# Kernel optimization log

Hardware: AMD Instinct MI355X
Metric: run time of the kernel (lower is better)

## Reference

```python
import jax, jax.numpy as jnp
import numpy as np
from jax import lax

B, F, T, H = 32, 1024, 512, 64
ENC_SIZES = [2*F+1, 1387, 726, H]      # linear interp 2049 -> 64, depth 3
DEC_SIZES = [F+H+1, 1067, 1046, F]     # linear interp 1089 -> 1024, depth 3


def _mlp(ws, bs, x):
    # fully connected stack, ReLU between layers, no final activation
    n = len(ws)
    for i in range(n):
        x = x @ ws[i] + bs[i]
        if i < n - 1:
            x = jax.nn.relu(x)
    return x


def setup_inputs() -> dict:
    key = jax.random.key(0)
    ks = jax.random.split(key, 8)
    d = {"x": jax.random.normal(ks[0], (B, F, T), dtype=jnp.float32)}
    for i, (fin, fout) in enumerate(zip(ENC_SIZES[:-1], ENC_SIZES[1:])):
        d[f"ew{i}"] = jax.random.normal(ks[1+i], (fin, fout), jnp.float32) / np.sqrt(fin)
        d[f"eb{i}"] = jnp.zeros((fout,), jnp.float32)
    for i, (fin, fout) in enumerate(zip(DEC_SIZES[:-1], DEC_SIZES[1:])):
        d[f"dw{i}"] = jax.random.normal(ks[4+i], (fin, fout), jnp.float32) / np.sqrt(fin)
        d[f"db{i}"] = jnp.zeros((fout,), jnp.float32)
    return d


def reference(x, ew0, eb0, ew1, eb1, ew2, eb2, dw0, db0, dw1, db1, dw2, db2):
    enc_w, enc_b = (ew0, ew1, ew2), (eb0, eb1, eb2)
    dec_w, dec_b = (dw0, dw1, dw2), (db0, db1, db2)
    b = x.shape[0]
    xs = jnp.moveaxis(x, 2, 0)                       # [T, B, F]
    ts = (jnp.arange(T, dtype=x.dtype) / T)          # [T]

    # ---- encode: prev_stft feedback recurrence ----
    def enc_step(prev_stft, inp):
        curr, tval = inp
        tcol = jnp.full((b, 1), tval, dtype=x.dtype)
        comb = jnp.concatenate([prev_stft, curr, tcol], axis=1)  # [B, 2F+1]
        h = _mlp(enc_w, enc_b, comb)                             # [B, H]
        return curr, h

    _, hs = lax.scan(enc_step, jnp.zeros((b, F), x.dtype), (xs, ts))
    # flatten(-2) then view(B,H,T) round-trips, so keep [T,B,H]; tanh applied after flatten
    hiddens = jnp.tanh(hs)                           # [T, B, H]

    # ---- decode: prev_stft = decoder output recurrence ----
    def dec_step(prev_stft, inp):
        h_t, tval = inp
        tcol = jnp.full((b, 1), tval, dtype=x.dtype)
        comb = jnp.concatenate([h_t, prev_stft, tcol], axis=1)   # [B, H+F+1]
        out = _mlp(dec_w, dec_b, comb)                           # [B, F]
        return out, out

    _, ys = lax.scan(dec_step, jnp.zeros((b, F), x.dtype), (hiddens, ts))
    return jnp.transpose(ys, (1, 2, 0))              # [B, F, T]
```

## Files before the change

### kernel.cpp

```cpp
#include <hip/hip_runtime.h>
#include <hip/hip_bf16.h>
#include <hip/hip_fp16.h>


typedef _Float16 f16x8 __attribute__((ext_vector_type(8)));
typedef float f32x4 __attribute__((ext_vector_type(4)));
typedef unsigned short u16;
typedef unsigned int u32;
typedef unsigned long long u64;

#define MFMA(a, b, c) __builtin_amdgcn_mfma_f32_16x16x32_f16((a), (b), (c), 0, 0, 0)

__device__ __forceinline__ float h2f(u16 u) { __half h; __builtin_memcpy(&h, &u, 2); return __half2float(h); }
__device__ __forceinline__ u16 f2h(float f) { __half h = __float2half(f); u16 u; __builtin_memcpy(&u, &h, 2); return u; }

__device__ __forceinline__ void st_act4(u32* p, u32 v) {
  __hip_atomic_store(p, v, __ATOMIC_RELAXED, __HIP_MEMORY_SCOPE_AGENT);
}
__device__ __forceinline__ f16x8 ld_act16(const u16* p) {
  u64 lo = __hip_atomic_load((const u64*)p, __ATOMIC_RELAXED, __HIP_MEMORY_SCOPE_AGENT);
  u64 hi = __hip_atomic_load((const u64*)(p + 4), __ATOMIC_RELAXED, __HIP_MEMORY_SCOPE_AGENT);
  union { u64 q[2]; f16x8 v; } u;
  u.q[0] = lo; u.q[1] = hi;
  return u.v;
}

__global__ __launch_bounds__(256) void zero_u16_kernel(u16* p, int n) {
  int i = blockIdx.x * 256 + threadIdx.x;
  if (i < n) p[i] = 0;
}
__global__ __launch_bounds__(256) void zero_u32_kernel(int* p, int n) {
  int i = blockIdx.x * 256 + threadIdx.x;
  if (i < n) p[i] = 0;
}
__global__ __launch_bounds__(256) void zpad_kernel(u16* p) {
  int id = blockIdx.x * 256 + threadIdx.x;
  int row = id >> 4, col = 1072 + (id & 15);
  p[(size_t)row * 1088 + col] = 0;
}

__global__ __launch_bounds__(256) void transpose_kernel(const float* __restrict__ x, u16* __restrict__ xT) {
  __shared__ float tile[64][65];
  int b = blockIdx.z, f0 = blockIdx.x * 64, t0 = blockIdx.y * 64;
  const float* xp = x + (size_t)b * (1024 * 512);
  for (int rep = 0; rep < 16; ++rep) {
    int e = rep * 256 + threadIdx.x;
    int fi = e >> 6, tj = e & 63;
    tile[fi][tj] = xp[(size_t)(f0 + fi) * 512 + t0 + tj];
  }
  __syncthreads();
  for (int rep = 0; rep < 16; ++rep) {
    int e = rep * 256 + threadIdx.x;
    int tj = e >> 6, fi = e & 63;
    xT[(size_t)((t0 + tj + 1) * 32 + b) * 1024 + f0 + fi] = f2h(tile[fi][tj]);
  }
}

__global__ __launch_bounds__(256) void pack_w_kernel(const float* __restrict__ W, int ldw, int row0,
                                                     int Kr, int Nr, u16* __restrict__ out, int Np, int total) {
  int id = blockIdx.x * 256 + threadIdx.x;
  if (id >= total) return;
  int kq = id / Np, n = id % Np;
  union { u16 v[8]; uint4 q; } un;
#pragma unroll
  for (int j = 0; j < 8; ++j) {
    int k = kq * 8 + j;
    float f = (k < Kr && n < Nr) ? W[(size_t)(row0 + k) * ldw + n] : 0.f;
    un.v[j] = f2h(f);
  }
  *(uint4*)(out + (size_t)id * 8) = un.q;
}

__global__ __launch_bounds__(256) void c2x_kernel(const float* __restrict__ dw0, const float* __restrict__ db2,
                                                  float* __restrict__ c2x) {
  int n = blockIdx.x * 256 + threadIdx.x;
  if (n >= 1152) return;
  float s = 0.f;
  if (n < 1067) {
    for (int k = 0; k < 1024; ++k) s += db2[k] * dw0[(size_t)(64 + k) * 1067 + n];
  }
  c2x[n] = s;
}

__global__ __launch_bounds__(256) void cvt_a_kernel(const float* __restrict__ src, u16* __restrict__ dst) {
  int i = blockIdx.x * 256 + threadIdx.x;
  int r = i >> 10;
  dst[i] = f2h(r < 1046 ? src[i] : 0.f);
}

template <int TWOSRC, int ACT, int T1, int T2, int PACKO>
__global__ __launch_bounds__(256) void gemm_kernel(
    const u16* __restrict__ A, int lda,
    const u16* __restrict__ Wp, int Np,
    const float* __restrict__ bias, int nb,
    const float* __restrict__ wt1, int nw1,
    const float* __restrict__ wt2, int nw2,
    u16* __restrict__ out, int ldo, int Kp) {
  __shared__ u16 As[128][72];
  __shared__ u16 Bs[8 * 64 * 8];
  const int tid = threadIdx.x;
  const int bx = blockIdx.x, by = blockIdx.y;
  const int m0 = by * 128, n0 = bx * 64;
  const int l = tid & 63, wv = tid >> 6, lm = l & 15, lg = l >> 4;
  f32x4 acc[2][4] = {};
  for (int k0 = 0; k0 < Kp; k0 += 64) {
#pragma unroll
    for (int c = 0; c < 4; ++c) {
      int idx = c * 256 + tid;
      int row = idx >> 3, seg = idx & 7;
      int kk = k0 + seg * 8;
      const u16* ap;
      if (TWOSRC) {
        int half = (kk >= 1024) ? 1 : 0;
        ap = A + (size_t)(m0 + row + half * 32) * lda + (kk - half * 1024);
      } else {
        ap = A + (size_t)(m0 + row) * lda + kk;
      }
      *(uint4*)&As[row][seg * 8] = *(const uint4*)ap;
    }
#pragma unroll
    for (int c = 0; c < 2; ++c) {
      int idx = c * 256 + tid;
      int e0 = idx * 8;
      int kq = e0 >> 9, inner = e0 & 511;
      const u16* gp = Wp + (size_t)((k0 >> 3) + kq) * (Np * 8) + n0 * 8 + inner;
      *(uint4*)(Bs + e0) = *(const uint4*)gp;
    }
    __syncthreads();
#pragma unroll
    for (int ks = 0; ks < 2; ++ks) {
      f16x8 af0 = *(const f16x8*)&As[wv * 32 + lm][ks * 32 + lg * 8];
      f16x8 af1 = *(const f16x8*)&As[wv * 32 + 16 + lm][ks * 32 + lg * 8];
#pragma unroll
      for (int nf = 0; nf < 4; ++nf) {
        f16x8 bfr = *(const f16x8*)(Bs + ((ks * 4 + lg) * 64 + nf * 16 + lm) * 8);
        acc[0][nf] = MFMA(af0, bfr, acc[0][nf]);
        acc[1][nf] = MFMA(af1, bfr, acc[1][nf]);
      }
    }
    __syncthreads();
  }
#pragma unroll
  for (int mr = 0; mr < 2; ++mr) {
    int rb = m0 + wv * 32 + mr * 16;
    int tt = rb >> 5;
#pragma unroll
    for (int nf = 0; nf < 4; ++nf) {
      int col = n0 + nf * 16 + lm;
      float bv = (col < nb) ? bias[col] : 0.f;
      if (T1) bv += (float)tt * (1.f / 512.f) * ((col < nw1) ? wt1[col] : 0.f);
      if (T2) bv += ((tt > 0) ? 1.f : 0.f) * ((col < nw2) ? wt2[col] : 0.f);
#pragma unroll
      for (int v = 0; v < 4; ++v) {
        float xv = acc[mr][nf][v] + bv;
        if (ACT == 1) xv = fmaxf(xv, 0.f);
        if (ACT == 2) xv = tanhf(xv);
        if (PACKO) {
          int r = rb + lg * 4 + v;
          out[((size_t)(r >> 3) * Np + col) * 8 + (r & 7)] = f2h(xv);
        } else {
          out[(size_t)(rb + lg * 4 + v) * ldo + col] = f2h(xv);
        }
      }
    }
  }
}

#define NWG 67

__device__ __forceinline__ void gbar(int* flags, int bid, int tid, int gen) {
  asm volatile("s_waitcnt vmcnt(0)" ::: "memory");
  __syncthreads();
  if (tid == 0)
    __hip_atomic_store(flags + bid * 32, gen, __ATOMIC_RELAXED, __HIP_MEMORY_SCOPE_AGENT);
  if (tid < NWG) {
    while (__hip_atomic_load(flags + tid * 32, __ATOMIC_RELAXED, __HIP_MEMORY_SCOPE_AGENT) < gen)
      __builtin_amdgcn_s_sleep(1);
  }
  __syncthreads();
}

__device__ __forceinline__ void dec_mm(const u16* __restrict__ in, const u16* wl,
                                       float (*red)[512], int tid, int lm, int lg, int wv,
                                       int e0, float& s0, float& s1) {
  const int kq0 = wv * 36;
  f32x4 acc0 = {}, acc1 = {};
#pragma unroll
  for (int ks = 0; ks < 9; ++ks) {
    int kq = kq0 + ks * 4 + lg;
    const u16* pa = in + kq * 256 + lm * 8;
    f16x8 a0f = ld_act16(pa);
    f16x8 a1f = ld_act16(pa + 128);
    f16x8 bf = *(const f16x8*)(wl + ((size_t)kq * 16 + lm) * 8);
    acc0 = MFMA(a0f, bf, acc0);
    acc1 = MFMA(a1f, bf, acc1);
  }
  __syncthreads();
#pragma unroll
  for (int v = 0; v < 4; ++v) {
    red[wv][(lg * 4 + v) * 16 + lm] = acc0[v];
    red[wv][(16 + lg * 4 + v) * 16 + lm] = acc1[v];
  }
  __syncthreads();
  s0 = red[0][e0] + red[1][e0] + red[2][e0] + red[3][e0];
  s1 = red[0][e0 + 1] + red[1][e0 + 1] + red[2][e0 + 1] + red[3][e0 + 1];
}

__global__ __launch_bounds__(256, 1) void decoder_kernel(
    const u16* __restrict__ W1p, const u16* __restrict__ Mp,
    const u16* __restrict__ hpart, const float* __restrict__ db1,
    u16* a0, u16* a1, u16* __restrict__ a1buf, int* flags) {
  __shared__ __align__(16) u16 wlds[2 * 2304 * 8];
  __shared__ float red[4][512];
  const int tid = threadIdx.x, bid = blockIdx.x;
  const int l = tid & 63, wv = tid >> 6, lm = l & 15, lg = l >> 4;
  const int n0 = bid * 16;
  for (int i = tid; i < 2 * 2304; i += 256) {
    int layer = i / 2304, rem = i % 2304, kq = rem >> 4, c = rem & 15;
    const u16* base = (layer == 0) ? W1p : Mp;
    *(uint4*)(wlds + (size_t)i * 8) = *(const uint4*)(base + ((size_t)kq * 1152 + n0 + c) * 8);
  }
  const int e0 = tid * 2, row = e0 >> 4, c0 = e0 & 15, na = n0 + c0;
  u32* a0slot = (u32*)(a0 + (((size_t)(na >> 3) * 32 + row) * 8 + (na & 7)));
  u32* a1slot = (u32*)(a1 + (((size_t)(na >> 3) * 32 + row) * 8 + (na & 7)));
  int gen = 0;
  {
    u32 pk = *(const u32*)(hpart + row * 1152 + na);
    float s0 = fmaxf(h2f((u16)(pk & 0xffff)), 0.f);
    float s1 = fmaxf(h2f((u16)(pk >> 16)), 0.f);
    st_act4(a0slot, (u32)f2h(s0) | ((u32)f2h(s1) << 16));
  }
  gbar(flags, bid, tid, ++gen);
#pragma unroll 1
  for (int t = 0; t < 512; ++t) {
    float bv0 = (na < 1046) ? db1[na] : 0.f;
    float bv1 = (na + 1 < 1046) ? db1[na + 1] : 0.f;
    float s0, s1;
    dec_mm(a0, wlds, red, tid, lm, lg, wv, e0, s0, s1);
    s0 = fmaxf(s0 + bv0, 0.f);
    s1 = fmaxf(s1 + bv1, 0.f);
    u32 opk = (u32)f2h(s0) | ((u32)f2h(s1) << 16);
    st_act4(a1slot, opk);
    __builtin_nontemporal_store(opk, (u32*)(a1buf + ((size_t)(t * 32 + row) * 1088 + na)));
    gbar(flags, bid, tid, ++gen);
    if (t < 511) {
      u32 pk = *(const u32*)(hpart + (size_t)(t + 1) * 36864 + row * 1152 + na);
      dec_mm(a1, wlds + 2304 * 8, red, tid, lm, lg, wv, e0, s0, s1);
      s0 = fmaxf(s0 + h2f((u16)(pk & 0xffff)), 0.f);
      s1 = fmaxf(s1 + h2f((u16)(pk >> 16)), 0.f);
      st_act4(a0slot, (u32)f2h(s0) | ((u32)f2h(s1) << 16));
      gbar(flags, bid, tid, ++gen);
    }
  }
}

__global__ __launch_bounds__(256) void finalize_kernel(const u16* __restrict__ ytmp,
                                                       float* __restrict__ dout) {
  __shared__ float tile[64][65];
  int b = blockIdx.z, n0 = blockIdx.x * 64, t0 = blockIdx.y * 64;
  for (int rep = 0; rep < 16; ++rep) {
    int e = rep * 256 + threadIdx.x;
    int tt = e >> 6, nn = e & 63;
    tile[tt][nn] = h2f(ytmp[(size_t)((t0 + tt) * 32 + b) * 1024 + n0 + nn]);
  }
  __syncthreads();
  for (int rep = 0; rep < 16; ++rep) {
    int e = rep * 256 + threadIdx.x;
    int nn = e >> 6, tt = e & 63;
    dout[((size_t)b * 1024 + n0 + nn) * 512 + t0 + tt] = tile[tt][nn];
  }
}

extern "C" void kernel_launch(void* const* d_in, const int* in_sizes, int n_in,
                              void* d_out, int out_size, void* d_ws, size_t ws_size,
                              hipStream_t stream) {
  (void)in_sizes; (void)n_in; (void)out_size; (void)ws_size;
  const float* x   = (const float*)d_in[0];
  const float* ew0 = (const float*)d_in[1];
  const float* eb0 = (const float*)d_in[2];
  const float* ew1 = (const float*)d_in[3];
  const float* eb1 = (const float*)d_in[4];
  const float* ew2 = (const float*)d_in[5];
  const float* eb2 = (const float*)d_in[6];
  const float* dw0 = (const float*)d_in[7];
  const float* db0 = (const float*)d_in[8];
  const float* dw1 = (const float*)d_in[9];
  const float* db1 = (const float*)d_in[10];
  const float* dw2 = (const float*)d_in[11];
  const float* db2 = (const float*)d_in[12];

  char* ws = (char*)d_ws;
  u16* xT    = (u16*)(ws + 0);
  u16* ytmp  = (u16*)(ws + 0);
  u16* act2  = (u16*)(ws + 33619968ull);
  u16* A16   = (u16*)(ws + 33619968ull);
  u16* Mp    = (u16*)(ws + 33619968ull + 2359296ull);
  int* flags = (int*)(ws + 33619968ull + 8388608ull);
  u16* hid   = (u16*)(ws + 58785792ull);
  u16* hpart = (u16*)(ws + 60882944ull);
  u16* We0p  = (u16*)(ws + 98631680ull);
  u16* We1p  = (u16*)(ws + 104398848ull);
  u16* We2p  = (u16*)(ws + 106561536ull);
  u16* Wh0p  = (u16*)(ws + 106659840ull);
  u16* Wd0p  = (u16*)(ws + 106807296ull);
  u16* Wd1p  = (u16*)(ws + 109461504ull);
  u16* Wd2p  = (u16*)(ws + 112115712ull);
  float* c2x = (float*)(ws + 114769920ull);
  u16* a0    = (u16*)(ws + 114774528ull);
  u16* a1    = (u16*)(ws + 114848256ull);

  u16* act1  = (u16*)d_out;
  u16* a1buf = (u16*)d_out;
  float* dout = (float*)d_out;

  zero_u16_kernel<<<dim3(128), dim3(256), 0, stream>>>(xT, 32 * 1024);
  zero_u16_kernel<<<dim3(288), dim3(256), 0, stream>>>(a0, 2 * 36864);

  transpose_kernel<<<dim3(16, 8, 32), dim3(256), 0, stream>>>(x, xT);

  pack_w_kernel<<<dim3(1408), dim3(256), 0, stream>>>(ew0, 1387, 0, 2048, 1387, We0p, 1408, 256 * 1408);
  pack_w_kernel<<<dim3(528),  dim3(256), 0, stream>>>(ew1, 726, 0, 1387, 726, We1p, 768, 176 * 768);
  pack_w_kernel<<<dim3(24),   dim3(256), 0, stream>>>(ew2, 64, 0, 726, 64, We2p, 64, 96 * 64);
  pack_w_kernel<<<dim3(36),   dim3(256), 0, stream>>>(dw0, 1067, 0, 64, 1067, Wh0p, 1152, 8 * 1152);
  pack_w_kernel<<<dim3(648),  dim3(256), 0, stream>>>(dw0, 1067, 64, 1024, 1067, Wd0p, 1152, 144 * 1152);
  pack_w_kernel<<<dim3(648),  dim3(256), 0, stream>>>(dw1, 1046, 0, 1067, 1046, Wd1p, 1152, 144 * 1152);
  pack_w_kernel<<<dim3(648),  dim3(256), 0, stream>>>(dw2, 1024, 0, 1046, 1024, Wd2p, 1152, 144 * 1152);

  c2x_kernel<<<dim3(5), dim3(256), 0, stream>>>(dw0, db2, c2x);

  gemm_kernel<1, 1, 1, 0, 0><<<dim3(22, 128), dim3(256), 0, stream>>>(
      xT, 1024, We0p, 1408, eb0, 1387, ew0 + (size_t)2048 * 1387, 1387, nullptr, 0, act1, 1408, 2048);
  gemm_kernel<0, 1, 0, 0, 0><<<dim3(12, 128), dim3(256), 0, stream>>>(
      act1, 1408, We1p, 768, eb1, 726, nullptr, 0, nullptr, 0, act2, 768, 1408);
  gemm_kernel<0, 2, 0, 0, 0><<<dim3(1, 128), dim3(256), 0, stream>>>(
      act2, 768, We2p, 64, eb2, 64, nullptr, 0, nullptr, 0, hid, 64, 768);
  gemm_kernel<0, 0, 1, 1, 0><<<dim3(18, 128), dim3(256), 0, stream>>>(
      hid, 64, Wh0p, 1152, db0, 1067, dw0 + (size_t)1088 * 1067, 1067, c2x, 1152, hpart, 1152, 64);

  cvt_a_kernel<<<dim3(4608), dim3(256), 0, stream>>>(dw2, A16);
  gemm_kernel<0, 0, 0, 0, 1><<<dim3(18, 9), dim3(256), 0, stream>>>(
      A16, 1024, Wd0p, 1152, nullptr, 0, nullptr, 0, nullptr, 0, Mp, 0, 1024);

  zero_u32_kernel<<<dim3(9), dim3(256), 0, stream>>>(flags, NWG * 32);
  zpad_kernel<<<dim3(1024), dim3(256), 0, stream>>>(a1buf);

  decoder_kernel<<<dim3(NWG), dim3(256), 0, stream>>>(Wd1p, Mp, hpart, db1, a0, a1, a1buf, flags);

  gemm_kernel<0, 0, 0, 0, 0><<<dim3(16, 128), dim3(256), 0, stream>>>(
      a1buf, 1088, Wd2p, 1152, db2, 1024, nullptr, 0, nullptr, 0, ytmp, 1024, 1088);
  finalize_kernel<<<dim3(16, 8, 32), dim3(256), 0, stream>>>(ytmp, dout);
}
```

Baseline: 3.766 ms.

## Split decoder recurrence into two independent batch-half chains with smaller barriers

The persistent decoder kernel now runs two independent chains, one per half of the batch (16 rows each), on 68 workgroups. Each workgroup handles 32 output columns instead of 16, and each chain synchronises only its own 34 workgroups through a separate flag set. This is meant to cut grid-barrier latency on the serial 512-step recurrence by shrinking each barrier's participant count, at the cost of more weight data per workgroup in LDS. The a1buf store is no longer nontemporal, and the zero-padding and activation-zeroing launches are removed. Removing those launches may leave padding columns 1072-1087 of a1buf or the activation buffers uninitialised.

```diff
diff --git a/kernel.cpp b/kernel.cpp
--- a/kernel.cpp
+++ b/kernel.cpp
@@ -32,11 +32,6 @@
 __global__ __launch_bounds__(256) void zero_u32_kernel(int* p, int n) {
   int i = blockIdx.x * 256 + threadIdx.x;
   if (i < n) p[i] = 0;
-}
-__global__ __launch_bounds__(256) void zpad_kernel(u16* p) {
-  int id = blockIdx.x * 256 + threadIdx.x;
-  int row = id >> 4, col = 1072 + (id & 15);
-  p[(size_t)row * 1088 + col] = 0;
 }
 
 __global__ __launch_bounds__(256) void transpose_kernel(const float* __restrict__ x, u16* __restrict__ xT) {
@@ -166,91 +161,99 @@
   }
 }
 
-#define NWG 67
-
-__device__ __forceinline__ void gbar(int* flags, int bid, int tid, int gen) {
+#define NWGD 68
+#define NWGC 34
+
+__device__ __forceinline__ void gbar(int* cf, int wgc, int tid, int gen) {
   asm volatile("s_waitcnt vmcnt(0)" ::: "memory");
   __syncthreads();
   if (tid == 0)
-    __hip_atomic_store(flags + bid * 32, gen, __ATOMIC_RELAXED, __HIP_MEMORY_SCOPE_AGENT);
-  if (tid < NWG) {
-    while (__hip_atomic_load(flags + tid * 32, __ATOMIC_RELAXED, __HIP_MEMORY_SCOPE_AGENT) < gen)
+    __hip_atomic_store(cf + wgc * 4, gen, __ATOMIC_RELAXED, __HIP_MEMORY_SCOPE_AGENT);
+  if (tid < NWGC) {
+    while (__hip_atomic_load(cf + tid * 4, __ATOMIC_RELAXED, __HIP_MEMORY_SCOPE_AGENT) < gen)
       __builtin_amdgcn_s_sleep(1);
   }
   __syncthreads();
 }
 
-__device__ __forceinline__ void dec_mm(const u16* __restrict__ in, const u16* wl,
-                                       float (*red)[512], int tid, int lm, int lg, int wv,
-                                       int e0, float& s0, float& s1) {
+__device__ __forceinline__ void dec_mm32(const u16* __restrict__ in, const u16* wl,
+                                         float (*red)[512], int lm, int lg, int wv) {
   const int kq0 = wv * 36;
-  f32x4 acc0 = {}, acc1 = {};
+  f32x4 accA = {}, accB = {};
 #pragma unroll
   for (int ks = 0; ks < 9; ++ks) {
     int kq = kq0 + ks * 4 + lg;
-    const u16* pa = in + kq * 256 + lm * 8;
-    f16x8 a0f = ld_act16(pa);
-    f16x8 a1f = ld_act16(pa + 128);
-    f16x8 bf = *(const f16x8*)(wl + ((size_t)kq * 16 + lm) * 8);
-    acc0 = MFMA(a0f, bf, acc0);
-    acc1 = MFMA(a1f, bf, acc1);
+    f16x8 af = ld_act16(in + (size_t)kq * 128 + lm * 8);
+    f16x8 b0 = *(const f16x8*)(wl + ((size_t)kq * 32 + lm) * 8);
+    f16x8 b1 = *(const f16x8*)(wl + ((size_t)kq * 32 + 16 + lm) * 8);
+    accA = MFMA(af, b0, accA);
+    accB = MFMA(af, b1, accB);
   }
   __syncthreads();
 #pragma unroll
   for (int v = 0; v < 4; ++v) {
-    red[wv][(lg * 4 + v) * 16 + lm] = acc0[v];
-    red[wv][(16 + lg * 4 + v) * 16 + lm] = acc1[v];
-  }
-  __syncthreads();
-  s0 = red[0][e0] + red[1][e0] + red[2][e0] + red[3][e0];
-  s1 = red[0][e0 + 1] + red[1][e0 + 1] + red[2][e0 + 1] + red[3][e0 + 1];
+    red[wv][(lg * 4 + v) * 32 + lm] = accA[v];
+    red[wv][(lg * 4 + v) * 32 + 16 + lm] = accB[v];
+  }
+  __syncthreads();
 }
 
 __global__ __launch_bounds__(256, 1) void decoder_kernel(
     const u16* __restrict__ W1p, const u16* __restrict__ Mp,
     const u16* __restrict__ hpart, const float* __restrict__ db1,
-    u16* a0, u16* a1, u16* __restrict__ a1buf, int* flags) {
-  __shared__ __align__(16) u16 wlds[2 * 2304 * 8];
+    u16* actbase, u16* __restrict__ a1buf, int* flags) {
+  __shared__ __align__(16) u16 w1lds[144 * 32 * 8];
+  __shared__ __align__(16) u16 mlds[144 * 32 * 8];
   __shared__ float red[4][512];
   const int tid = threadIdx.x, bid = blockIdx.x;
+  const int chain = bid & 1, wgc = bid >> 1;
+  const int n0 = wgc * 32;
   const int l = tid & 63, wv = tid >> 6, lm = l & 15, lg = l >> 4;
-  const int n0 = bid * 16;
-  for (int i = tid; i < 2 * 2304; i += 256) {
-    int layer = i / 2304, rem = i % 2304, kq = rem >> 4, c = rem & 15;
-    const u16* base = (layer == 0) ? W1p : Mp;
-    *(uint4*)(wlds + (size_t)i * 8) = *(const uint4*)(base + ((size_t)kq * 1152 + n0 + c) * 8);
-  }
-  const int e0 = tid * 2, row = e0 >> 4, c0 = e0 & 15, na = n0 + c0;
-  u32* a0slot = (u32*)(a0 + (((size_t)(na >> 3) * 32 + row) * 8 + (na & 7)));
-  u32* a1slot = (u32*)(a1 + (((size_t)(na >> 3) * 32 + row) * 8 + (na & 7)));
+  for (int i = tid; i < 144 * 32; i += 256) {
+    int kq = i >> 5, c = i & 31;
+    *(uint4*)(w1lds + (size_t)i * 8) = *(const uint4*)(W1p + ((size_t)kq * 1152 + n0 + c) * 8);
+    *(uint4*)(mlds + (size_t)i * 8) = *(const uint4*)(Mp + ((size_t)kq * 1152 + n0 + c) * 8);
+  }
+  u16* a0 = actbase + (size_t)chain * 2 * 18432;
+  u16* a1 = a0 + 18432;
+  int* cf = flags + chain * 512;
+  const int e0 = tid * 2;
+  const int erow = e0 >> 5, ecol = e0 & 31;
+  const int na = n0 + ecol;
+  const int hrow = chain * 16 + erow;
+  u32* a0slot = (u32*)(a0 + ((size_t)(na >> 3) * 128 + (size_t)erow * 8 + (na & 7)));
+  u32* a1slot = (u32*)(a1 + ((size_t)(na >> 3) * 128 + (size_t)erow * 8 + (na & 7)));
+  const float bv0 = (na < 1046) ? db1[na] : 0.f;
+  const float bv1 = (na + 1 < 1046) ? db1[na + 1] : 0.f;
   int gen = 0;
+  __syncthreads();
   {
-    u32 pk = *(const u32*)(hpart + row * 1152 + na);
+    u32 pk = *(const u32*)(hpart + (size_t)hrow * 1152 + na);
     float s0 = fmaxf(h2f((u16)(pk & 0xffff)), 0.f);
     float s1 = fmaxf(h2f((u16)(pk >> 16)), 0.f);
     st_act4(a0slot, (u32)f2h(s0) | ((u32)f2h(s1) << 16));
   }
-  gbar(flags, bid, tid, ++gen);
+  gbar(cf, wgc, tid, ++gen);
 #pragma unroll 1
   for (int t = 0; t < 512; ++t) {
-    float bv0 = (na < 1046) ? db1[na] : 0.f;
-    float bv1 = (na + 1 < 1046) ? db1[na + 1] : 0.f;
-    float s0, s1;
-    dec_mm(a0, wlds, red, tid, lm, lg, wv, e0, s0, s1);
-    s0 = fmaxf(s0 + bv0, 0.f);
-    s1 = fmaxf(s1 + bv1, 0.f);
+    dec_mm32(a0, w1lds, red, lm, lg, wv);
+    float s0 = red[0][e0] + red[1][e0] + red[2][e0] + red[3][e0] + bv0;
+    float s1 = red[0][e0 + 1] + red[1][e0 + 1] + red[2][e0 + 1] + red[3][e0 + 1] + bv1;
+    s0 = fmaxf(s0, 0.f);
+    s1 = fmaxf(s1, 0.f);
     u32 opk = (u32)f2h(s0) | ((u32)f2h(s1) << 16);
     st_act4(a1slot, opk);
-    __builtin_nontemporal_store(opk, (u32*)(a1buf + ((size_t)(t * 32 + row) * 1088 + na)));
-    gbar(flags, bid, tid, ++gen);
-    if (t < 511) {
-      u32 pk = *(const u32*)(hpart + (size_t)(t + 1) * 36864 + row * 1152 + na);
-      dec_mm(a1, wlds + 2304 * 8, red, tid, lm, lg, wv, e0, s0, s1);
-      s0 = fmaxf(s0 + h2f((u16)(pk & 0xffff)), 0.f);
-      s1 = fmaxf(s1 + h2f((u16)(pk >> 16)), 0.f);
-      st_act4(a0slot, (u32)f2h(s0) | ((u32)f2h(s1) << 16));
-      gbar(flags, bid, tid, ++gen);
-    }
+    *(u32*)(a1buf + ((size_t)(t * 32 + hrow) * 1088 + na)) = opk;
+    u32 hpk = 0;
+    if (t < 511)
+      hpk = *(const u32*)(hpart + (size_t)(t + 1) * 36864 + (size_t)hrow * 1152 + na);
+    gbar(cf, wgc, tid, ++gen);
+    if (t == 511) break;
+    dec_mm32(a1, mlds, red, lm, lg, wv);
+    float r0 = red[0][e0] + red[1][e0] + red[2][e0] + red[3][e0] + h2f((u16)(hpk & 0xffff));
+    float r1 = red[0][e0 + 1] + red[1][e0 + 1] + red[2][e0 + 1] + red[3][e0 + 1] + h2f((u16)(hpk >> 16));
+    st_act4(a0slot, (u32)f2h(fmaxf(r0, 0.f)) | ((u32)f2h(fmaxf(r1, 0.f)) << 16));
+    gbar(cf, wgc, tid, ++gen);
   }
 }
 
@@ -306,15 +309,13 @@
   u16* Wd1p  = (u16*)(ws + 109461504ull);
   u16* Wd2p  = (u16*)(ws + 112115712ull);
   float* c2x = (float*)(ws + 114769920ull);
-  u16* a0    = (u16*)(ws + 114774528ull);
-  u16* a1    = (u16*)(ws + 114848256ull);
+  u16* actb  = (u16*)(ws + 114774528ull);
 
   u16* act1  = (u16*)d_out;
   u16* a1buf = (u16*)d_out;
   float* dout = (float*)d_out;
 
   zero_u16_kernel<<<dim3(128), dim3(256), 0, stream>>>(xT, 32 * 1024);
-  zero_u16_kernel<<<dim3(288), dim3(256), 0, stream>>>(a0, 2 * 36864);
 
   transpose_kernel<<<dim3(16, 8, 32), dim3(256), 0, stream>>>(x, xT);
 
@@ -341,10 +342,9 @@
   gemm_kernel<0, 0, 0, 0, 1><<<dim3(18, 9), dim3(256), 0, stream>>>(
       A16, 1024, Wd0p, 1152, nullptr, 0, nullptr, 0, nullptr, 0, Mp, 0, 1024);
 
-  zero_u32_kernel<<<dim3(9), dim3(256), 0, stream>>>(flags, NWG * 32);
-  zpad_kernel<<<dim3(1024), dim3(256), 0, stream>>>(a1buf);
-
-  decoder_kernel<<<dim3(NWG), dim3(256), 0, stream>>>(Wd1p, Mp, hpart, db1, a0, a1, a1buf, flags);
+  zero_u32_kernel<<<dim3(4), dim3(256), 0, stream>>>(flags, 2 * 512);
+
+  decoder_kernel<<<dim3(NWGD), dim3(256), 0, stream>>>(Wd1p, Mp, hpart, db1, actb, a1buf, flags);
 
   gemm_kernel<0, 0, 0, 0, 0><<<dim3(16, 128), dim3(256), 0, stream>>>(
       a1buf, 1088, Wd2p, 1152, db2, 1024, nullptr, 0, nullptr, 0, ytmp, 1024, 1088);
```

After: 4.006 ms. 1.06x slower.

## Merge prep kernels and redesign decoder grid barrier with per-wave flags

Applied to the files above, without the earlier changes.

Merges the weight packing, zeroing and c2x kernels into one prep launch to cut launch overhead. Rewrites the decoder's inter-workgroup barrier so each wave publishes its own flag and spins on 64-bit loads, with no pre-barrier __syncthreads and no sleep. It also removes a __syncthreads in dec_mm, hoists the bias loads, prefetches the next hpart value before the matmul, and makes the a1buf store a regular store instead of nontemporal. The barrier gives up after a bounded number of spins, and dropping the sync before the reduction-buffer writes could race, so correctness depends on timing.

```diff
diff --git a/kernel.cpp b/kernel.cpp
--- a/kernel.cpp
+++ b/kernel.cpp
@@ -25,18 +25,61 @@
   return u.v;
 }
 
-__global__ __launch_bounds__(256) void zero_u16_kernel(u16* p, int n) {
-  int i = blockIdx.x * 256 + threadIdx.x;
-  if (i < n) p[i] = 0;
-}
-__global__ __launch_bounds__(256) void zero_u32_kernel(int* p, int n) {
-  int i = blockIdx.x * 256 + threadIdx.x;
-  if (i < n) p[i] = 0;
-}
-__global__ __launch_bounds__(256) void zpad_kernel(u16* p) {
-  int id = blockIdx.x * 256 + threadIdx.x;
-  int row = id >> 4, col = 1072 + (id & 15);
-  p[(size_t)row * 1088 + col] = 0;
+__device__ __forceinline__ void pack_body(const float* __restrict__ W, int ldw, int row0,
+                                          int Kr, int Nr, u16* __restrict__ out, int Np,
+                                          int id, int total) {
+  if (id >= total) return;
+  int kq = id / Np, n = id % Np;
+  union { u16 v[8]; uint4 q; } un;
+#pragma unroll
+  for (int j = 0; j < 8; ++j) {
+    int k = kq * 8 + j;
+    float f = (k < Kr && n < Nr) ? W[(size_t)(row0 + k) * ldw + n] : 0.f;
+    un.v[j] = f2h(f);
+  }
+  *(uint4*)(out + (size_t)id * 8) = un.q;
+}
+
+__global__ __launch_bounds__(256) void prep_kernel(
+    const float* __restrict__ ew0, const float* __restrict__ ew1, const float* __restrict__ ew2,
+    const float* __restrict__ dw0, const float* __restrict__ dw1, const float* __restrict__ dw2,
+    const float* __restrict__ db2,
+    u16* We0p, u16* We1p, u16* We2p, u16* Wh0p, u16* Wd0p, u16* Wd1p, u16* Wd2p,
+    u16* xT, float* c2x, int* flags, u16* acts) {
+  const int b = blockIdx.x, tid = threadIdx.x;
+  if (b < 1408) {
+    pack_body(ew0, 1387, 0, 2048, 1387, We0p, 1408, b * 256 + tid, 256 * 1408);
+  } else if (b < 1936) {
+    pack_body(ew1, 726, 0, 1387, 726, We1p, 768, (b - 1408) * 256 + tid, 176 * 768);
+  } else if (b < 1960) {
+    pack_body(ew2, 64, 0, 726, 64, We2p, 64, (b - 1936) * 256 + tid, 96 * 64);
+  } else if (b < 1996) {
+    pack_body(dw0, 1067, 0, 64, 1067, Wh0p, 1152, (b - 1960) * 256 + tid, 8 * 1152);
+  } else if (b < 2644) {
+    pack_body(dw0, 1067, 64, 1024, 1067, Wd0p, 1152, (b - 1996) * 256 + tid, 144 * 1152);
+  } else if (b < 3292) {
+    pack_body(dw1, 1046, 0, 1067, 1046, Wd1p, 1152, (b - 2644) * 256 + tid, 144 * 1152);
+  } else if (b < 3940) {
+    pack_body(dw2, 1024, 0, 1046, 1024, Wd2p, 1152, (b - 3292) * 256 + tid, 144 * 1152);
+  } else if (b < 4068) {
+    int i = (b - 3940) * 256 + tid;
+    if (i < 32768) xT[i] = 0;
+  } else if (b < 4073) {
+    int n = (b - 4068) * 256 + tid;
+    if (n < 1152) {
+      float s = 0.f;
+      if (n < 1067) {
+        for (int k = 0; k < 1024; ++k) s += db2[k] * dw0[(size_t)(64 + k) * 1067 + n];
+      }
+      c2x[n] = s;
+    }
+  } else if (b < 4078) {
+    int i = (b - 4073) * 256 + tid;
+    if (i < 1072) flags[i] = 0;
+  } else {
+    int i = (b - 4078) * 256 + tid;
+    if (i < 9216) { uint4 z = {}; *(uint4*)(acts + (size_t)i * 8) = z; }
+  }
 }
 
 __global__ __launch_bounds__(256) void transpose_kernel(const float* __restrict__ x, u16* __restrict__ xT) {
@@ -56,36 +99,16 @@
   }
 }
 
-__global__ __launch_bounds__(256) void pack_w_kernel(const float* __restrict__ W, int ldw, int row0,
-                                                     int Kr, int Nr, u16* __restrict__ out, int Np, int total) {
-  int id = blockIdx.x * 256 + threadIdx.x;
-  if (id >= total) return;
-  int kq = id / Np, n = id % Np;
-  union { u16 v[8]; uint4 q; } un;
-#pragma unroll
-  for (int j = 0; j < 8; ++j) {
-    int k = kq * 8 + j;
-    float f = (k < Kr && n < Nr) ? W[(size_t)(row0 + k) * ldw + n] : 0.f;
-    un.v[j] = f2h(f);
-  }
-  *(uint4*)(out + (size_t)id * 8) = un.q;
-}
-
-__global__ __launch_bounds__(256) void c2x_kernel(const float* __restrict__ dw0, const float* __restrict__ db2,
-                                                  float* __restrict__ c2x) {
-  int n = blockIdx.x * 256 + threadIdx.x;
-  if (n >= 1152) return;
-  float s = 0.f;
-  if (n < 1067) {
-    for (int k = 0; k < 1024; ++k) s += db2[k] * dw0[(size_t)(64 + k) * 1067 + n];
-  }
-  c2x[n] = s;
-}
-
 __global__ __launch_bounds__(256) void cvt_a_kernel(const float* __restrict__ src, u16* __restrict__ dst) {
   int i = blockIdx.x * 256 + threadIdx.x;
   int r = i >> 10;
   dst[i] = f2h(r < 1046 ? src[i] : 0.f);
+}
+
+__global__ __launch_bounds__(256) void zpad_kernel(u16* p) {
+  int id = blockIdx.x * 256 + threadIdx.x;
+  int row = id >> 4, col = 1072 + (id & 15);
+  p[(size_t)row * 1088 + col] = 0;
 }
 
 template <int TWOSRC, int ACT, int T1, int T2, int PACKO>
@@ -168,14 +191,23 @@
 
 #define NWG 67
 
-__device__ __forceinline__ void gbar(int* flags, int bid, int tid, int gen) {
+__device__ __forceinline__ void gbar(int* flags, int bid, int wv, int l, int gen) {
   asm volatile("s_waitcnt vmcnt(0)" ::: "memory");
-  __syncthreads();
-  if (tid == 0)
-    __hip_atomic_store(flags + bid * 32, gen, __ATOMIC_RELAXED, __HIP_MEMORY_SCOPE_AGENT);
-  if (tid < NWG) {
-    while (__hip_atomic_load(flags + tid * 32, __ATOMIC_RELAXED, __HIP_MEMORY_SCOPE_AGENT) < gen)
-      __builtin_amdgcn_s_sleep(1);
+  if (l == 0)
+    __hip_atomic_store(flags + bid * 16 + wv, gen, __ATOMIC_RELAXED, __HIP_MEMORY_SCOPE_AGENT);
+  int wg = wv + l * 4;
+  if (l < 17 && wg < NWG) {
+    const u64* p = (const u64*)(flags + wg * 16);
+    int it = 0;
+    for (;;) {
+      u64 ab = __hip_atomic_load(p, __ATOMIC_RELAXED, __HIP_MEMORY_SCOPE_AGENT);
+      u64 cd = __hip_atomic_load(p + 1, __ATOMIC_RELAXED, __HIP_MEMORY_SCOPE_AGENT);
+      int a = (int)ab, b2 = (int)(ab >> 32), c = (int)cd, d = (int)(cd >> 32);
+      int m = a < b2 ? a : b2;
+      int m2 = c < d ? c : d;
+      if ((m < m2 ? m : m2) >= gen) break;
+      if (++it >= (1 << 16)) break;
+    }
   }
   __syncthreads();
 }
@@ -195,7 +227,6 @@
     acc0 = MFMA(a0f, bf, acc0);
     acc1 = MFMA(a1f, bf, acc1);
   }
-  __syncthreads();
 #pragma unroll
   for (int v = 0; v < 4; ++v) {
     red[wv][(lg * 4 + v) * 16 + lm] = acc0[v];
@@ -223,34 +254,35 @@
   const int e0 = tid * 2, row = e0 >> 4, c0 = e0 & 15, na = n0 + c0;
   u32* a0slot = (u32*)(a0 + (((size_t)(na >> 3) * 32 + row) * 8 + (na & 7)));
   u32* a1slot = (u32*)(a1 + (((size_t)(na >> 3) * 32 + row) * 8 + (na & 7)));
+  const float bv0 = (na < 1046) ? db1[na] : 0.f;
+  const float bv1 = (na + 1 < 1046) ? db1[na + 1] : 0.f;
   int gen = 0;
+  __syncthreads();
   {
     u32 pk = *(const u32*)(hpart + row * 1152 + na);
     float s0 = fmaxf(h2f((u16)(pk & 0xffff)), 0.f);
     float s1 = fmaxf(h2f((u16)(pk >> 16)), 0.f);
     st_act4(a0slot, (u32)f2h(s0) | ((u32)f2h(s1) << 16));
   }
-  gbar(flags, bid, tid, ++gen);
+  gbar(flags, bid, wv, l, ++gen);
 #pragma unroll 1
   for (int t = 0; t < 512; ++t) {
-    float bv0 = (na < 1046) ? db1[na] : 0.f;
-    float bv1 = (na + 1 < 1046) ? db1[na + 1] : 0.f;
+    u32 hpk = 0;
+    if (t < 511) hpk = *(const u32*)(hpart + (size_t)(t + 1) * 36864 + row * 1152 + na);
     float s0, s1;
     dec_mm(a0, wlds, red, tid, lm, lg, wv, e0, s0, s1);
     s0 = fmaxf(s0 + bv0, 0.f);
     s1 = fmaxf(s1 + bv1, 0.f);
     u32 opk = (u32)f2h(s0) | ((u32)f2h(s1) << 16);
     st_act4(a1slot, opk);
-    __builtin_nontemporal_store(opk, (u32*)(a1buf + ((size_t)(t * 32 + row) * 1088 + na)));
-    gbar(flags, bid, tid, ++gen);
-    if (t < 511) {
-      u32 pk = *(const u32*)(hpart + (size_t)(t + 1) * 36864 + row * 1152 + na);
-      dec_mm(a1, wlds + 2304 * 8, red, tid, lm, lg, wv, e0, s0, s1);
-      s0 = fmaxf(s0 + h2f((u16)(pk & 0xffff)), 0.f);
-      s1 = fmaxf(s1 + h2f((u16)(pk >> 16)), 0.f);
-      st_act4(a0slot, (u32)f2h(s0) | ((u32)f2h(s1) << 16));
-      gbar(flags, bid, tid, ++gen);
-    }
+    *(u32*)(a1buf + ((size_t)(t * 32 + row) * 1088 + na)) = opk;
+    gbar(flags, bid, wv, l, ++gen);
+    if (t == 511) break;
+    dec_mm(a1, wlds + 2304 * 8, red, tid, lm, lg, wv, e0, s0, s1);
+    s0 = fmaxf(s0 + h2f((u16)(hpk & 0xffff)), 0.f);
+    s1 = fmaxf(s1 + h2f((u16)(hpk >> 16)), 0.f);
+    st_act4(a0slot, (u32)f2h(s0) | ((u32)f2h(s1) << 16));
+    gbar(flags, bid, wv, l, ++gen);
   }
 }
 
@@ -295,7 +327,6 @@
   u16* act2  = (u16*)(ws + 33619968ull);
   u16* A16   = (u16*)(ws + 33619968ull);
   u16* Mp    = (u16*)(ws + 33619968ull + 2359296ull);
-  int* flags = (int*)(ws + 33619968ull + 8388608ull);
   u16* hid   = (u16*)(ws + 58785792ull);
   u16* hpart = (u16*)(ws + 60882944ull);
   u16* We0p  = (u16*)(ws + 98631680ull);
@@ -308,25 +339,17 @@
   float* c2x = (float*)(ws + 114769920ull);
   u16* a0    = (u16*)(ws + 114774528ull);
   u16* a1    = (u16*)(ws + 114848256ull);
+  int* flags = (int*)(ws + 114921984ull);
 
   u16* act1  = (u16*)d_out;
   u16* a1buf = (u16*)d_out;
   float* dout = (float*)d_out;
 
-  zero_u16_kernel<<<dim3(128), dim3(256), 0, stream>>>(xT, 32 * 1024);
-  zero_u16_kernel<<<dim3(288), dim3(256), 0, stream>>>(a0, 2 * 36864);
+  prep_kernel<<<dim3(4114), dim3(256), 0, stream>>>(
+      ew0, ew1, ew2, dw0, dw1, dw2, db2,
+      We0p, We1p, We2p, Wh0p, Wd0p, Wd1p, Wd2p, xT, c2x, flags, a0);
 
   transpose_kernel<<<dim3(16, 8, 32), dim3(256), 0, stream>>>(x, xT);
-
-  pack_w_kernel<<<dim3(1408), dim3(256), 0, stream>>>(ew0, 1387, 0, 2048, 1387, We0p, 1408, 256 * 1408);
-  pack_w_kernel<<<dim3(528),  dim3(256), 0, stream>>>(ew1, 726, 0, 1387, 726, We1p, 768, 176 * 768);
-  pack_w_kernel<<<dim3(24),   dim3(256), 0, stream>>>(ew2, 64, 0, 726, 64, We2p, 64, 96 * 64);
-  pack_w_kernel<<<dim3(36),   dim3(256), 0, stream>>>(dw0, 1067, 0, 64, 1067, Wh0p, 1152, 8 * 1152);
-  pack_w_kernel<<<dim3(648),  dim3(256), 0, stream>>>(dw0, 1067, 64, 1024, 1067, Wd0p, 1152, 144 * 1152);
-  pack_w_kernel<<<dim3(648),  dim3(256), 0, stream>>>(dw1, 1046, 0, 1067, 1046, Wd1p, 1152, 144 * 1152);
-  pack_w_kernel<<<dim3(648),  dim3(256), 0, stream>>>(dw2, 1024, 0, 1046, 1024, Wd2p, 1152, 144 * 1152);
-
-  c2x_kernel<<<dim3(5), dim3(256), 0, stream>>>(dw0, db2, c2x);
 
   gemm_kernel<1, 1, 1, 0, 0><<<dim3(22, 128), dim3(256), 0, stream>>>(
       xT, 1024, We0p, 1408, eb0, 1387, ew0 + (size_t)2048 * 1387, 1387, nullptr, 0, act1, 1408, 2048);
@@ -341,7 +364,6 @@
   gemm_kernel<0, 0, 0, 0, 1><<<dim3(18, 9), dim3(256), 0, stream>>>(
       A16, 1024, Wd0p, 1152, nullptr, 0, nullptr, 0, nullptr, 0, Mp, 0, 1024);
 
-  zero_u32_kernel<<<dim3(9), dim3(256), 0, stream>>>(flags, NWG * 32);
   zpad_kernel<<<dim3(1024), dim3(256), 0, stream>>>(a1buf);
 
   decoder_kernel<<<dim3(NWG), dim3(256), 0, stream>>>(Wd1p, Mp, hpart, db1, a0, a1, a1buf, flags);
```

New measurement: 4.644 ms. 23.3% more time.
